# Optimization experiments

Hardware: AMD Instinct MI355X
Metric: run time of the kernel (lower is better)

## Reference

```python
import jax, jax.numpy as jnp
import numpy as np

N_NODES = 50000
N_EDGES = 1600000
IN_DIM = 128
OUT_DIM = 32
N_HEADS = 4


def setup_inputs() -> dict:
    key = jax.random.key(0)
    k_x, k_e, k_w, k_a = jax.random.split(key, 4)
    x = jax.random.normal(k_x, (N_NODES, IN_DIM), dtype=jnp.float32)
    edge_index = jax.random.randint(k_e, (N_EDGES, 2), 0, N_NODES, dtype=jnp.int64)
    # Xavier-uniform-like init scales
    w_bound = np.sqrt(6.0 / (IN_DIM + OUT_DIM)).astype(np.float32)
    a_bound = np.sqrt(6.0 / (N_HEADS + 2 * OUT_DIM)).astype(np.float32)
    weight = jax.random.uniform(k_w, (N_HEADS, IN_DIM, OUT_DIM), dtype=jnp.float32,
                                minval=-w_bound, maxval=w_bound)
    attn = jax.random.uniform(k_a, (N_HEADS, 2 * OUT_DIM), dtype=jnp.float32,
                              minval=-a_bound, maxval=a_bound)
    return {"x": x, "edge_index": edge_index, "weight": weight, "attn": attn}


def reference(x, edge_index, weight, attn):
    # x: [N, in_dim]; edge_index: [E, 2]; weight: [H, in, out]; attn: [H, 2*out]
    num_nodes = x.shape[0]
    out_dim = weight.shape[2]
    src = edge_index[:, 0]
    dst = edge_index[:, 1]

    # Per-head linear transform: [N, H, out]
    Wh = jnp.einsum('ni,hio->nho', x, weight)
    Wh_src = Wh[src]  # [E, H, out]
    Wh_dst = Wh[dst]  # [E, H, out]

    a_src = attn[:, :out_dim]   # [H, out]
    a_dst = attn[:, out_dim:]   # [H, out]
    # Edge scores: [E, H]
    e = jnp.einsum('eho,ho->eh', Wh_src, a_src) + jnp.einsum('eho,ho->eh', Wh_dst, a_dst)
    e = jax.nn.leaky_relu(e, negative_slope=0.2)

    # Segment softmax over incoming edges of each dst node
    max_per_dst = jax.ops.segment_max(e, dst, num_segments=num_nodes)  # [N, H]
    max_per_dst = jnp.where(jnp.isfinite(max_per_dst), max_per_dst, 0.0)
    exp_e = jnp.exp(e - max_per_dst[dst])                               # [E, H]
    sum_per_dst = jax.ops.segment_sum(exp_e, dst, num_segments=num_nodes)  # [N, H]
    alpha = exp_e / (sum_per_dst[dst] + 1e-9)                           # [E, H]
    # Dropout is identity in eval mode.

    # Weighted scatter-add aggregation: [N, H, out]
    out = jax.ops.segment_sum(alpha[:, :, None] * Wh_src, dst, num_segments=num_nodes)
    h = out.reshape(num_nodes, -1)  # concat heads -> [N, H*out]
    return h, alpha
```

## Files before the change

### kernel.cpp

```cpp
#include <hip/hip_runtime.h>
#include <hip/hip_bf16.h>
#include <math.h>

#define N_NODES 50000
#define N_EDGES 1600000
#define IN_DIM  128
#define OUT_DIM 32
#define N_HEADS 4
#define WH_DIM  (N_HEADS * OUT_DIM)
#define CAP     128
#define NB_SCAN 196
#define NPASS   4
#define WIN     (N_NODES / NPASS)
#define NCHUNK  32
#define CE      (N_EDGES / NCHUNK)

typedef __attribute__((ext_vector_type(8))) short short8;
typedef __attribute__((ext_vector_type(4))) float floatx4;

__device__ __forceinline__ short f2bf(float v) {
    __hip_bfloat16 b = __float2bfloat16(v);
    return *reinterpret_cast<short*>(&b);
}
__device__ __forceinline__ float lrelu(float v) {
    return v > 0.0f ? v : 0.2f * v;
}

__device__ __forceinline__ void load_edge(const void* eidx, int is32, int e,
                                          int& s, int& d) {
    if (is32) {
        const int2 v = ((const int2*)eidx)[e];
        s = v.x; d = v.y;
    } else {
        const longlong2 v = ((const longlong2*)eidx)[e];
        s = (int)v.x; d = (int)v.y;
    }
}

__global__ void k_detect(const int* __restrict__ eidx, int* __restrict__ flag) {
    int i = threadIdx.x;
    int r = eidx[2 * (i * (N_EDGES / 256)) + 1];
    if (r != 0) atomicOr(flag, 1);
}

__global__ __launch_bounds__(256) void k_cvt(
        const void* __restrict__ eidx, const int* __restrict__ flag,
        int* __restrict__ s32, int* __restrict__ d32) {
    int e = blockIdx.x * 256 + threadIdx.x;
    if (e >= N_EDGES) return;
    int s, d;
    load_edge(eidx, *flag, e, s, d);
    s32[e] = s;
    d32[e] = d;
}

__global__ __launch_bounds__(256) void k_wh(
        const float* __restrict__ x, const float* __restrict__ weight,
        const float* __restrict__ attn,
        __hip_bfloat16* __restrict__ Wh16, float* __restrict__ sb16) {
    __shared__ float ubuf[128 * 8];
    __shared__ short xsw[4 * 4 * 64 * 8];
    __shared__ short bsw[4 * 9 * 64 * 8];
    const int t  = threadIdx.x;
    const int nb = blockIdx.x * 64;

    {
        int c = t & 7, k0 = t >> 3;
        int h = c & 3;
        const float* ap = attn + h * 64 + (c >> 2) * 32;
        for (int k = k0; k < 128; k += 32) {
            const float* wp = weight + h * (IN_DIM * OUT_DIM) + k * OUT_DIM;
            float u = 0.f;
#pragma unroll
            for (int o = 0; o < 32; o += 4) {
                float4 wv = *(const float4*)(wp + o);
                float4 av = *(const float4*)(ap + o);
                u += wv.x * av.x + wv.y * av.y + wv.z * av.z + wv.w * av.w;
            }
            ubuf[k * 8 + c] = u;
        }
    }
    __syncthreads();

    for (int f = t; f < 128 * 128; f += 256) {
        int k = f >> 7, c = f & 127;
        float w = weight[(c >> 5) * (IN_DIM * OUT_DIM) + k * OUT_DIM + (c & 31)];
        int kc = k >> 5, quad = (k >> 3) & 3, j = k & 7;
        bsw[((kc * 9 + (c >> 4)) * 64 + quad * 16 + (c & 15)) * 8 + j] = f2bf(w);
    }
    for (int f = t; f < 128 * 16; f += 256) {
        int k = f >> 4, c = f & 15;
        float w = (c < 8) ? ubuf[k * 8 + c] : 0.f;
        int kc = k >> 5, quad = (k >> 3) & 3, j = k & 7;
        bsw[((kc * 9 + 8) * 64 + quad * 16 + c) * 8 + j] = f2bf(w);
    }
    for (int f = t; f < 64 * 32; f += 256) {
        int n = f >> 5, k = (f & 31) * 4;
        int ng = nb + n; if (ng > N_NODES - 1) ng = N_NODES - 1;
        float4 v = *(const float4*)(x + (size_t)ng * IN_DIM + k);
        int wg = n >> 4, m = n & 15, kc = k >> 5, quad = (k >> 3) & 3, j = k & 7;
        short4 sv = make_short4(f2bf(v.x), f2bf(v.y), f2bf(v.z), f2bf(v.w));
        *(short4*)&xsw[(((wg * 4 + kc) * 64) + quad * 16 + m) * 8 + j] = sv;
    }
    __syncthreads();

    const int wg = t >> 6, lane = t & 63;
    floatx4 acc[9];
#pragma unroll
    for (int i = 0; i < 9; ++i) acc[i] = (floatx4){0.f, 0.f, 0.f, 0.f};
#pragma unroll
    for (int kc = 0; kc < 4; ++kc) {
        short8 a = *(short8*)&xsw[((wg * 4 + kc) * 64 + lane) * 8];
#pragma unroll
        for (int cg = 0; cg < 9; ++cg) {
            short8 b = *(short8*)&bsw[((kc * 9 + cg) * 64 + lane) * 8];
            acc[cg] = __builtin_amdgcn_mfma_f32_16x16x32_bf16(a, b, acc[cg],
                                                              0, 0, 0);
        }
    }

    const int col = lane & 15, quad = lane >> 4;
#pragma unroll
    for (int r = 0; r < 4; ++r) {
        int n = nb + wg * 16 + quad * 4 + r;
        if (n >= N_NODES) continue;
#pragma unroll
        for (int cg = 0; cg < 8; ++cg)
            Wh16[(size_t)n * WH_DIM + cg * 16 + col] =
                __float2bfloat16(acc[cg][r]);
        if (col < 8) sb16[(size_t)n * 16 + col] = acc[8][r];
    }
}

__global__ __launch_bounds__(1024) void k_hist(
        const int* __restrict__ d32, int* __restrict__ hist) {
    __shared__ int hbin[WIN];
    const int c = blockIdx.x, w = blockIdx.y;
    for (int i = threadIdx.x; i < WIN; i += 1024) hbin[i] = 0;
    __syncthreads();
    const int w0 = w * WIN;
    for (int e = c * CE + threadIdx.x; e < (c + 1) * CE; e += 1024) {
        unsigned u = (unsigned)(d32[e] - w0);
        if (u < WIN) atomicAdd(&hbin[u], 1);
    }
    __syncthreads();
    for (int i = threadIdx.x; i < WIN; i += 1024)
        hist[c * N_NODES + w0 + i] = hbin[i];
}

__global__ __launch_bounds__(256) void k_scan1(
        const int* __restrict__ hist, int* __restrict__ pre,
        int* __restrict__ bsum) {
    __shared__ int sh[256];
    const int t = threadIdx.x;
    const int i = blockIdx.x * 256 + t;
    int v = 0;
    if (i < N_NODES)
        for (int c = 0; c < NCHUNK; ++c) v += hist[c * N_NODES + i];
    sh[t] = v;
    __syncthreads();
    for (int d = 1; d < 256; d <<= 1) {
        int u = (t >= d) ? sh[t - d] : 0;
        __syncthreads();
        sh[t] += u;
        __syncthreads();
    }
    if (i < N_NODES) pre[i] = sh[t] - v;
    if (t == 255) bsum[blockIdx.x] = sh[255];
}

__global__ __launch_bounds__(256) void k_scan2(
        const int* __restrict__ bsum, int* __restrict__ bbase) {
    __shared__ int sh[256];
    const int t = threadIdx.x;
    int v = (t < NB_SCAN) ? bsum[t] : 0;
    sh[t] = v;
    __syncthreads();
    for (int d = 1; d < 256; d <<= 1) {
        int u = (t >= d) ? sh[t - d] : 0;
        __syncthreads();
        sh[t] += u;
        __syncthreads();
    }
    if (t < NB_SCAN) bbase[t] = sh[t] - v;
}

__global__ __launch_bounds__(256) void k_base(
        const int* __restrict__ pre, const int* __restrict__ bbase,
        int* __restrict__ hist) {
    int d = blockIdx.x * 256 + threadIdx.x;
    if (d >= N_NODES) return;
    int run = pre[d] + bbase[d >> 8];
    for (int c = 0; c < NCHUNK; ++c) {
        int t0 = hist[c * N_NODES + d];
        hist[c * N_NODES + d] = run;
        run += t0;
    }
}

__global__ __launch_bounds__(1024) void k_scatter(
        const int* __restrict__ s32, const int* __restrict__ d32,
        const int* __restrict__ hist, int* __restrict__ csr) {
    __shared__ int pos[WIN];
    const int c = blockIdx.x, w = blockIdx.y;
    const int w0 = w * WIN;
    for (int i = threadIdx.x; i < WIN; i += 1024)
        pos[i] = hist[c * N_NODES + w0 + i];
    __syncthreads();
    for (int e = c * CE + threadIdx.x; e < (c + 1) * CE; e += 1024) {
        unsigned u = (unsigned)(d32[e] - w0);
        if (u < WIN) {
            int p = atomicAdd(&pos[u], 1);
            csr[p] = s32[e];
        }
    }
}

__global__ __launch_bounds__(256) void k_node(
        const int* __restrict__ pre, const int* __restrict__ bbase,
        const int* __restrict__ csr, float* __restrict__ sb16,
        const __hip_bfloat16* __restrict__ Wh16,
        float* __restrict__ out_h) {
    __shared__ int    sbuf[4][CAP];
    __shared__ float4 e4b[4][CAP];
    const int wv = threadIdx.x >> 6;
    const int t  = threadIdx.x & 63;
    const int n  = blockIdx.x * 4 + wv;
    const int beg = pre[n] + bbase[n >> 8];
    const int end = (n + 1 < N_NODES) ? pre[n + 1] + bbase[(n + 1) >> 8]
                                      : N_EDGES;
    const int deg = end - beg;

    const float4 sd = *(const float4*)(sb16 + (size_t)n * 16 + 4);

    float4 sum = {0.f, 0.f, 0.f, 0.f};
    for (int l = t; l < deg; l += 64) {
        int s = csr[beg + l];
        float4 ss = *(const float4*)(sb16 + (size_t)s * 16);
        float4 ex;
        ex.x = __expf(lrelu(ss.x + sd.x));
        ex.y = __expf(lrelu(ss.y + sd.y));
        ex.z = __expf(lrelu(ss.z + sd.z));
        ex.w = __expf(lrelu(ss.w + sd.w));
        if (l < CAP) { sbuf[wv][l] = s; e4b[wv][l] = ex; }
        sum.x += ex.x; sum.y += ex.y; sum.z += ex.z; sum.w += ex.w;
    }
#pragma unroll
    for (int o = 32; o; o >>= 1) {
        sum.x += __shfl_xor(sum.x, o);
        sum.y += __shfl_xor(sum.y, o);
        sum.z += __shfl_xor(sum.z, o);
        sum.w += __shfl_xor(sum.w, o);
    }
    float4 inv;
    inv.x = 1.0f / (sum.x + 1e-9f); inv.y = 1.0f / (sum.y + 1e-9f);
    inv.z = 1.0f / (sum.z + 1e-9f); inv.w = 1.0f / (sum.w + 1e-9f);
    if (t == 0) *(float4*)(sb16 + (size_t)n * 16 + 8) = inv;

    const int h = t >> 4;
    const float invh = (h == 0) ? inv.x : (h == 1) ? inv.y
                     : (h == 2) ? inv.z : inv.w;
    float2 acc = {0.0f, 0.0f};
    if (deg <= CAP) {
        int j = 0;
        for (; j + 3 < deg; j += 4) {
            int s0 = sbuf[wv][j],     s1 = sbuf[wv][j + 1];
            int s2 = sbuf[wv][j + 2], s3 = sbuf[wv][j + 3];
            float a0 = ((const float*)&e4b[wv][j])[h]     * invh;
            float a1 = ((const float*)&e4b[wv][j + 1])[h] * invh;
            float a2 = ((const float*)&e4b[wv][j + 2])[h] * invh;
            float a3 = ((const float*)&e4b[wv][j + 3])[h] * invh;
            __hip_bfloat162 w0 = ((const __hip_bfloat162*)(Wh16 + (size_t)s0 * WH_DIM))[t];
            __hip_bfloat162 w1 = ((const __hip_bfloat162*)(Wh16 + (size_t)s1 * WH_DIM))[t];
            __hip_bfloat162 w2 = ((const __hip_bfloat162*)(Wh16 + (size_t)s2 * WH_DIM))[t];
            __hip_bfloat162 w3 = ((const __hip_bfloat162*)(Wh16 + (size_t)s3 * WH_DIM))[t];
            float2 f0 = __bfloat1622float2(w0);
            float2 f1 = __bfloat1622float2(w1);
            float2 f2 = __bfloat1622float2(w2);
            float2 f3 = __bfloat1622float2(w3);
            acc.x += a0 * f0.x + a1 * f1.x + a2 * f2.x + a3 * f3.x;
            acc.y += a0 * f0.y + a1 * f1.y + a2 * f2.y + a3 * f3.y;
        }
        for (; j < deg; ++j) {
            int s0 = sbuf[wv][j];
            float a0 = ((const float*)&e4b[wv][j])[h] * invh;
            __hip_bfloat162 w0 = ((const __hip_bfloat162*)(Wh16 + (size_t)s0 * WH_DIM))[t];
            float2 f0 = __bfloat1622float2(w0);
            acc.x += a0 * f0.x;
            acc.y += a0 * f0.y;
        }
    } else {
        float dh = (h == 0) ? sd.x : (h == 1) ? sd.y : (h == 2) ? sd.z : sd.w;
        for (int j = 0; j < deg; ++j) {
            int s0; float a0;
            if (j < CAP) {
                s0 = sbuf[wv][j];
                a0 = ((const float*)&e4b[wv][j])[h] * invh;
            } else {
                s0 = csr[beg + j];
                float sh = sb16[(size_t)s0 * 16 + h];
                a0 = __expf(lrelu(sh + dh)) * invh;
            }
            __hip_bfloat162 w0 = ((const __hip_bfloat162*)(Wh16 + (size_t)s0 * WH_DIM))[t];
            float2 f0 = __bfloat1622float2(w0);
            acc.x += a0 * f0.x;
            acc.y += a0 * f0.y;
        }
    }
    *(float2*)(out_h + (size_t)n * WH_DIM + 2 * t) = acc;
}

__global__ __launch_bounds__(256) void k_alpha(
        const int* __restrict__ s32, const int* __restrict__ d32,
        const float* __restrict__ sb16, float* __restrict__ ebuf) {
    int e = blockIdx.x * 256 + threadIdx.x;
    if (e >= N_EDGES) return;
    int s = s32[e], d = d32[e];
    float4 ss = *(const float4*)(sb16 + (size_t)s * 16);
    float4 sd = *(const float4*)(sb16 + (size_t)d * 16 + 4);
    float4 iv = *(const float4*)(sb16 + (size_t)d * 16 + 8);
    float4 a;
    a.x = __expf(lrelu(ss.x + sd.x)) * iv.x;
    a.y = __expf(lrelu(ss.y + sd.y)) * iv.y;
    a.z = __expf(lrelu(ss.z + sd.z)) * iv.z;
    a.w = __expf(lrelu(ss.w + sd.w)) * iv.w;
    *(float4*)(ebuf + (size_t)e * 4) = a;
}

extern "C" void kernel_launch(void* const* d_in, const int* in_sizes, int n_in,
                              void* d_out, int out_size, void* d_ws, size_t ws_size,
                              hipStream_t stream) {
    const float* x      = (const float*)d_in[0];
    const void*  eidx   = d_in[1];
    const float* weight = (const float*)d_in[2];
    const float* attn   = (const float*)d_in[3];

    float* out   = (float*)d_out;
    float* out_h = out;
    float* ebuf  = out + (size_t)N_NODES * WH_DIM;

    char* ws = (char*)d_ws;
    int*   flag  = (int*)ws;
    int*   bsum  = (int*)(ws + 64);
    int*   bbase = (int*)(ws + 896);
    int*   pre   = (int*)(ws + 2048);
    int*   s32   = (int*)(ws + 202112);
    int*   d32   = (int*)(ws + 6602112);
    int*   hist  = (int*)(ws + 13002112);
    int*   csr   = (int*)(ws + 19402112);
    __hip_bfloat16* Wh16 = (__hip_bfloat16*)(ws + 25802112);
    float* sb16  = (float*)(ws + 38602112);

    hipMemsetAsync(flag, 0, 4, stream);

    k_detect<<<1, 256, 0, stream>>>((const int*)eidx, flag);
    k_cvt<<<(N_EDGES + 255) / 256, 256, 0, stream>>>(eidx, flag, s32, d32);
    k_wh<<<(N_NODES + 63) / 64, 256, 0, stream>>>(x, weight, attn, Wh16, sb16);
    dim3 hg(NCHUNK, NPASS);
    k_hist<<<hg, 1024, 0, stream>>>(d32, hist);
    k_scan1<<<NB_SCAN, 256, 0, stream>>>(hist, pre, bsum);
    k_scan2<<<1, 256, 0, stream>>>(bsum, bbase);
    k_base<<<NB_SCAN, 256, 0, stream>>>(pre, bbase, hist);
    k_scatter<<<hg, 1024, 0, stream>>>(s32, d32, hist, csr);
    k_node<<<N_NODES / 4, 256, 0, stream>>>(pre, bbase, csr, sb16,
                                            Wh16, out_h);
    k_alpha<<<(N_EDGES + 255) / 256, 256, 0, stream>>>(s32, d32, sb16, ebuf);
}
```

Baseline: 284.3 us.

## Build CSR with global atomics and vectorize node aggregation across edges

Replaces the chunked shared-memory histogram and windowed scatter with a global atomic degree count fused into the edge conversion kernel, plus a single atomic-offset scatter. The exclusive-scan base computation is merged into the second scan kernel, and the index-width detection moves inside the conversion kernel. The node aggregation kernel now has 16-lane groups each handle a different edge with 16-byte bf16 loads, followed by a cross-group shuffle reduction. This cuts kernel launches and passes over the edge list. In exchange it relies on contended global atomics and gives a nondeterministic CSR order.

Result: slower. 428.4 us (+50.7%).

```diff
diff --git a/kernel.cpp b/kernel.cpp
--- a/kernel.cpp
+++ b/kernel.cpp
@@ -10,10 +10,6 @@
 #define WH_DIM  (N_HEADS * OUT_DIM)
 #define CAP     128
 #define NB_SCAN 196
-#define NPASS   4
-#define WIN     (N_NODES / NPASS)
-#define NCHUNK  32
-#define CE      (N_EDGES / NCHUNK)
 
 typedef __attribute__((ext_vector_type(8))) short short8;
 typedef __attribute__((ext_vector_type(4))) float floatx4;
@@ -37,21 +33,25 @@
     }
 }
 
-__global__ void k_detect(const int* __restrict__ eidx, int* __restrict__ flag) {
-    int i = threadIdx.x;
-    int r = eidx[2 * (i * (N_EDGES / 256)) + 1];
-    if (r != 0) atomicOr(flag, 1);
-}
-
 __global__ __launch_bounds__(256) void k_cvt(
-        const void* __restrict__ eidx, const int* __restrict__ flag,
-        int* __restrict__ s32, int* __restrict__ d32) {
-    int e = blockIdx.x * 256 + threadIdx.x;
+        const void* __restrict__ eidx,
+        int* __restrict__ s32, int* __restrict__ d32, int* __restrict__ deg) {
+    __shared__ int s_is32;
+    const int t = threadIdx.x;
+    if (t < 64) {
+        int hi = ((const int*)eidx)[2 * (t * 25000) + 1];
+        unsigned long long b = __ballot(hi != 0);
+        if (t == 0) s_is32 = (b != 0ULL) ? 1 : 0;
+    }
+    __syncthreads();
+    const int is32 = s_is32;
+    const int e = blockIdx.x * 256 + t;
     if (e >= N_EDGES) return;
     int s, d;
-    load_edge(eidx, *flag, e, s, d);
+    load_edge(eidx, is32, e, s, d);
     s32[e] = s;
     d32[e] = d;
+    atomicAdd(&deg[d], 1);
 }
 
 __global__ __launch_bounds__(256) void k_wh(
@@ -132,31 +132,13 @@
     }
 }
 
-__global__ __launch_bounds__(1024) void k_hist(
-        const int* __restrict__ d32, int* __restrict__ hist) {
-    __shared__ int hbin[WIN];
-    const int c = blockIdx.x, w = blockIdx.y;
-    for (int i = threadIdx.x; i < WIN; i += 1024) hbin[i] = 0;
-    __syncthreads();
-    const int w0 = w * WIN;
-    for (int e = c * CE + threadIdx.x; e < (c + 1) * CE; e += 1024) {
-        unsigned u = (unsigned)(d32[e] - w0);
-        if (u < WIN) atomicAdd(&hbin[u], 1);
-    }
-    __syncthreads();
-    for (int i = threadIdx.x; i < WIN; i += 1024)
-        hist[c * N_NODES + w0 + i] = hbin[i];
-}
-
 __global__ __launch_bounds__(256) void k_scan1(
-        const int* __restrict__ hist, int* __restrict__ pre,
+        const int* __restrict__ deg, int* __restrict__ pre,
         int* __restrict__ bsum) {
     __shared__ int sh[256];
     const int t = threadIdx.x;
     const int i = blockIdx.x * 256 + t;
-    int v = 0;
-    if (i < N_NODES)
-        for (int c = 0; c < NCHUNK; ++c) v += hist[c * N_NODES + i];
+    int v = (i < N_NODES) ? deg[i] : 0;
     sh[t] = v;
     __syncthreads();
     for (int d = 1; d < 256; d <<= 1) {
@@ -169,8 +151,9 @@
     if (t == 255) bsum[blockIdx.x] = sh[255];
 }
 
-__global__ __launch_bounds__(256) void k_scan2(
-        const int* __restrict__ bsum, int* __restrict__ bbase) {
+__global__ __launch_bounds__(256) void k_scan2off(
+        const int* __restrict__ bsum, int* __restrict__ bbase,
+        const int* __restrict__ pre, int* __restrict__ off) {
     __shared__ int sh[256];
     const int t = threadIdx.x;
     int v = (t < NB_SCAN) ? bsum[t] : 0;
@@ -182,38 +165,20 @@
         sh[t] += u;
         __syncthreads();
     }
-    if (t < NB_SCAN) bbase[t] = sh[t] - v;
-}
-
-__global__ __launch_bounds__(256) void k_base(
-        const int* __restrict__ pre, const int* __restrict__ bbase,
-        int* __restrict__ hist) {
-    int d = blockIdx.x * 256 + threadIdx.x;
-    if (d >= N_NODES) return;
-    int run = pre[d] + bbase[d >> 8];
-    for (int c = 0; c < NCHUNK; ++c) {
-        int t0 = hist[c * N_NODES + d];
-        hist[c * N_NODES + d] = run;
-        run += t0;
-    }
-}
-
-__global__ __launch_bounds__(1024) void k_scatter(
+    const int b = blockIdx.x;
+    const int exb = sh[b] - bsum[b];
+    if (t == 0) bbase[b] = exb;
+    const int i = b * 256 + t;
+    if (i < N_NODES) off[i] = pre[i] + exb;
+}
+
+__global__ __launch_bounds__(256) void k_scatter2(
         const int* __restrict__ s32, const int* __restrict__ d32,
-        const int* __restrict__ hist, int* __restrict__ csr) {
-    __shared__ int pos[WIN];
-    const int c = blockIdx.x, w = blockIdx.y;
-    const int w0 = w * WIN;
-    for (int i = threadIdx.x; i < WIN; i += 1024)
-        pos[i] = hist[c * N_NODES + w0 + i];
-    __syncthreads();
-    for (int e = c * CE + threadIdx.x; e < (c + 1) * CE; e += 1024) {
-        unsigned u = (unsigned)(d32[e] - w0);
-        if (u < WIN) {
-            int p = atomicAdd(&pos[u], 1);
-            csr[p] = s32[e];
-        }
-    }
+        int* __restrict__ off, int* __restrict__ csr) {
+    const int e = blockIdx.x * 256 + threadIdx.x;
+    if (e >= N_EDGES) return;
+    const int p = atomicAdd(&off[d32[e]], 1);
+    csr[p] = s32[e];
 }
 
 __global__ __launch_bounds__(256) void k_node(
@@ -257,57 +222,55 @@
     inv.z = 1.0f / (sum.z + 1e-9f); inv.w = 1.0f / (sum.w + 1e-9f);
     if (t == 0) *(float4*)(sb16 + (size_t)n * 16 + 8) = inv;
 
-    const int h = t >> 4;
+    const int esl = t >> 4;
+    const int dsl = t & 15;
+    const int h   = dsl >> 2;
     const float invh = (h == 0) ? inv.x : (h == 1) ? inv.y
                      : (h == 2) ? inv.z : inv.w;
-    float2 acc = {0.0f, 0.0f};
-    if (deg <= CAP) {
-        int j = 0;
-        for (; j + 3 < deg; j += 4) {
-            int s0 = sbuf[wv][j],     s1 = sbuf[wv][j + 1];
-            int s2 = sbuf[wv][j + 2], s3 = sbuf[wv][j + 3];
-            float a0 = ((const float*)&e4b[wv][j])[h]     * invh;
-            float a1 = ((const float*)&e4b[wv][j + 1])[h] * invh;
-            float a2 = ((const float*)&e4b[wv][j + 2])[h] * invh;
-            float a3 = ((const float*)&e4b[wv][j + 3])[h] * invh;
-            __hip_bfloat162 w0 = ((const __hip_bfloat162*)(Wh16 + (size_t)s0 * WH_DIM))[t];
-            __hip_bfloat162 w1 = ((const __hip_bfloat162*)(Wh16 + (size_t)s1 * WH_DIM))[t];
-            __hip_bfloat162 w2 = ((const __hip_bfloat162*)(Wh16 + (size_t)s2 * WH_DIM))[t];
-            __hip_bfloat162 w3 = ((const __hip_bfloat162*)(Wh16 + (size_t)s3 * WH_DIM))[t];
-            float2 f0 = __bfloat1622float2(w0);
-            float2 f1 = __bfloat1622float2(w1);
-            float2 f2 = __bfloat1622float2(w2);
-            float2 f3 = __bfloat1622float2(w3);
-            acc.x += a0 * f0.x + a1 * f1.x + a2 * f2.x + a3 * f3.x;
-            acc.y += a0 * f0.y + a1 * f1.y + a2 * f2.y + a3 * f3.y;
+    const float sdh  = (h == 0) ? sd.x : (h == 1) ? sd.y
+                     : (h == 2) ? sd.z : sd.w;
+    float acc0 = 0.f, acc1 = 0.f, acc2 = 0.f, acc3 = 0.f;
+    float acc4 = 0.f, acc5 = 0.f, acc6 = 0.f, acc7 = 0.f;
+    for (int jb = 0; jb < deg; jb += 4) {
+        const int idx = jb + esl;
+        float a = 0.f;
+        int s = sbuf[wv][0];
+        if (idx < deg) {
+            if (idx < CAP) {
+                s = sbuf[wv][idx];
+                a = ((const float*)&e4b[wv][idx])[h];
+            } else {
+                s = csr[beg + idx];
+                a = __expf(lrelu(sb16[(size_t)s * 16 + h] + sdh));
+            }
         }
-        for (; j < deg; ++j) {
-            int s0 = sbuf[wv][j];
-            float a0 = ((const float*)&e4b[wv][j])[h] * invh;
-            __hip_bfloat162 w0 = ((const __hip_bfloat162*)(Wh16 + (size_t)s0 * WH_DIM))[t];
-            float2 f0 = __bfloat1622float2(w0);
-            acc.x += a0 * f0.x;
-            acc.y += a0 * f0.y;
-        }
-    } else {
-        float dh = (h == 0) ? sd.x : (h == 1) ? sd.y : (h == 2) ? sd.z : sd.w;
-        for (int j = 0; j < deg; ++j) {
-            int s0; float a0;
-            if (j < CAP) {
-                s0 = sbuf[wv][j];
-                a0 = ((const float*)&e4b[wv][j])[h] * invh;
-            } else {
-                s0 = csr[beg + j];
-                float sh = sb16[(size_t)s0 * 16 + h];
-                a0 = __expf(lrelu(sh + dh)) * invh;
-            }
-            __hip_bfloat162 w0 = ((const __hip_bfloat162*)(Wh16 + (size_t)s0 * WH_DIM))[t];
-            float2 f0 = __bfloat1622float2(w0);
-            acc.x += a0 * f0.x;
-            acc.y += a0 * f0.y;
-        }
-    }
-    *(float2*)(out_h + (size_t)n * WH_DIM + 2 * t) = acc;
+        const uint4 w = *(const uint4*)(Wh16 + (size_t)s * WH_DIM + dsl * 8);
+        float f0 = __uint_as_float(w.x << 16);
+        float f1 = __uint_as_float(w.x & 0xffff0000u);
+        float f2 = __uint_as_float(w.y << 16);
+        float f3 = __uint_as_float(w.y & 0xffff0000u);
+        float f4 = __uint_as_float(w.z << 16);
+        float f5 = __uint_as_float(w.z & 0xffff0000u);
+        float f6 = __uint_as_float(w.w << 16);
+        float f7 = __uint_as_float(w.w & 0xffff0000u);
+        acc0 += a * f0; acc1 += a * f1; acc2 += a * f2; acc3 += a * f3;
+        acc4 += a * f4; acc5 += a * f5; acc6 += a * f6; acc7 += a * f7;
+    }
+    acc0 += __shfl_xor(acc0, 16); acc0 += __shfl_xor(acc0, 32);
+    acc1 += __shfl_xor(acc1, 16); acc1 += __shfl_xor(acc1, 32);
+    acc2 += __shfl_xor(acc2, 16); acc2 += __shfl_xor(acc2, 32);
+    acc3 += __shfl_xor(acc3, 16); acc3 += __shfl_xor(acc3, 32);
+    acc4 += __shfl_xor(acc4, 16); acc4 += __shfl_xor(acc4, 32);
+    acc5 += __shfl_xor(acc5, 16); acc5 += __shfl_xor(acc5, 32);
+    acc6 += __shfl_xor(acc6, 16); acc6 += __shfl_xor(acc6, 32);
+    acc7 += __shfl_xor(acc7, 16); acc7 += __shfl_xor(acc7, 32);
+    if (t < 16) {
+        float* op = out_h + (size_t)n * WH_DIM + dsl * 8;
+        float4 o0 = {acc0 * invh, acc1 * invh, acc2 * invh, acc3 * invh};
+        float4 o1 = {acc4 * invh, acc5 * invh, acc6 * invh, acc7 * invh};
+        *(float4*)op = o0;
+        *(float4*)(op + 4) = o1;
+    }
 }
 
 __global__ __launch_bounds__(256) void k_alpha(
@@ -340,28 +303,24 @@
     float* ebuf  = out + (size_t)N_NODES * WH_DIM;
 
     char* ws = (char*)d_ws;
-    int*   flag  = (int*)ws;
-    int*   bsum  = (int*)(ws + 64);
-    int*   bbase = (int*)(ws + 896);
-    int*   pre   = (int*)(ws + 2048);
-    int*   s32   = (int*)(ws + 202112);
-    int*   d32   = (int*)(ws + 6602112);
-    int*   hist  = (int*)(ws + 13002112);
-    int*   csr   = (int*)(ws + 19402112);
-    __hip_bfloat16* Wh16 = (__hip_bfloat16*)(ws + 25802112);
-    float* sb16  = (float*)(ws + 38602112);
-
-    hipMemsetAsync(flag, 0, 4, stream);
-
-    k_detect<<<1, 256, 0, stream>>>((const int*)eidx, flag);
-    k_cvt<<<(N_EDGES + 255) / 256, 256, 0, stream>>>(eidx, flag, s32, d32);
+    int*   bsum  = (int*)ws;
+    int*   bbase = (int*)(ws + 1024);
+    int*   deg   = (int*)(ws + 2048);
+    int*   pre   = (int*)(ws + 202112);
+    int*   off   = (int*)(ws + 402176);
+    int*   s32   = (int*)(ws + 602176);
+    int*   d32   = (int*)(ws + 7002176);
+    int*   csr   = (int*)(ws + 13402176);
+    __hip_bfloat16* Wh16 = (__hip_bfloat16*)(ws + 19802176);
+    float* sb16  = (float*)(ws + 32602176);
+
+    hipMemsetAsync(deg, 0, N_NODES * sizeof(int), stream);
+
+    k_cvt<<<(N_EDGES + 255) / 256, 256, 0, stream>>>(eidx, s32, d32, deg);
     k_wh<<<(N_NODES + 63) / 64, 256, 0, stream>>>(x, weight, attn, Wh16, sb16);
-    dim3 hg(NCHUNK, NPASS);
-    k_hist<<<hg, 1024, 0, stream>>>(d32, hist);
-    k_scan1<<<NB_SCAN, 256, 0, stream>>>(hist, pre, bsum);
-    k_scan2<<<1, 256, 0, stream>>>(bsum, bbase);
-    k_base<<<NB_SCAN, 256, 0, stream>>>(pre, bbase, hist);
-    k_scatter<<<hg, 1024, 0, stream>>>(s32, d32, hist, csr);
+    k_scan1<<<NB_SCAN, 256, 0, stream>>>(deg, pre, bsum);
+    k_scan2off<<<NB_SCAN, 256, 0, stream>>>(bsum, bbase, pre, off);
+    k_scatter2<<<(N_EDGES + 255) / 256, 256, 0, stream>>>(s32, d32, off, csr);
     k_node<<<N_NODES / 4, 256, 0, stream>>>(pre, bbase, csr, sb16,
                                             Wh16, out_h);
     k_alpha<<<(N_EDGES + 255) / 256, 256, 0, stream>>>(s32, d32, sb16, ebuf);
```
